# Performance work log

Measured on AMD Instinct MI355X. Metric: run time of the kernel, lower is better.

## Reference

```python
import jax, jax.numpy as jnp
import numpy as np

VOCAB = 101
EMB = 32
HID = 32


def setup_inputs() -> dict:
    key = jax.random.key(0)
    k = jax.random.split(key, 7)
    B, T = 4096, 512
    x = jax.random.randint(k[0], (B, T), 0, VOCAB, dtype=jnp.int32)
    emb = jax.random.normal(k[1], (VOCAB, EMB), dtype=jnp.float32) * 0.1
    # gate order: i, f, g, o (concatenated along last dim)
    Wx = jax.random.normal(k[2], (EMB, 4 * HID), dtype=jnp.float32) * 0.1
    Wh = jax.random.normal(k[3], (HID, 4 * HID), dtype=jnp.float32) * 0.1
    b = jax.random.normal(k[4], (4 * HID,), dtype=jnp.float32) * 0.1
    W_fc = jax.random.normal(k[5], (HID, 2), dtype=jnp.float32) * 0.1
    b_fc = jax.random.normal(k[6], (2,), dtype=jnp.float32) * 0.1
    return {"x": x, "emb": emb, "Wx": Wx, "Wh": Wh, "b": b, "W_fc": W_fc, "b_fc": b_fc}


def _lstm_last_h(xe, Wx, Wh, b):
    # xe: [B, T, EMB]
    B = xe.shape[0]
    # precompute input contributions for all timesteps: [T, B, 4H]
    xg = jnp.einsum('bte,eh->tbh', xe, Wx) + b
    h0 = jnp.zeros((B, HID), xe.dtype)
    c0 = jnp.zeros((B, HID), xe.dtype)

    def step(carry, xt):
        h, c = carry
        g = xt + h @ Wh  # [B, 4H]
        i, f, gg, o = jnp.split(g, 4, axis=-1)
        c = jax.nn.sigmoid(f) * c + jax.nn.sigmoid(i) * jnp.tanh(gg)
        h = jax.nn.sigmoid(o) * jnp.tanh(c)
        return (h, c), None

    (h, c), _ = jax.lax.scan(step, (h0, c0), xg)
    return h  # last hidden state == hidden_seq[:, -1, :]


def reference(x, emb, Wx, Wh, b, W_fc, b_fc):
    xe = emb[x]  # [B, T, EMB]
    h = _lstm_last_h(xe, Wx, Wh, b)
    return h @ W_fc + b_fc  # [B, 2]
```

## Files before the change

kernel.cpp:

```cpp
#include <hip/hip_runtime.h>
#include <stdint.h>

#define T_LEN 512
#define VOCAB 101
#define GSP   140
#define XPB   516
#define HPW   20
#define HB1   (16 * HPW)

typedef short short8 __attribute__((ext_vector_type(8)));
typedef short s16x4  __attribute__((ext_vector_type(4)));
typedef float f32x4  __attribute__((ext_vector_type(4)));

#define LOG2E 1.442695041f
#define L2E2  2.885390082f

__device__ __forceinline__ float asF(uint32_t u) {
    union { uint32_t i; float f; } x; x.i = u; return x.f;
}
__device__ __forceinline__ float bf2f(uint16_t u) { return asF(((uint32_t)u) << 16); }
__device__ __forceinline__ float bf_lo(uint32_t u) { return asF(u << 16); }
__device__ __forceinline__ float bf_hi(uint32_t u) { return asF(u & 0xFFFF0000u); }
__device__ __forceinline__ uint16_t f2bf(float f) {
    union { float f; uint32_t i; } x; x.f = f;
    return (uint16_t)((x.i + 0x7FFFu + ((x.i >> 16) & 1u)) >> 16);
}
__device__ __forceinline__ float getw(const void* p, int i, bool isbf) {
    return isbf ? bf2f(((const uint16_t*)p)[i]) : ((const float*)p)[i];
}
__device__ __forceinline__ bool detect_bf16(const void* embp) {
    const uint16_t* u = (const uint16_t*)embp;
    int sane = 0;
    for (int i = 0; i < 64; ++i) {
        uint16_t v = u[i];
        int e = (v >> 7) & 0xFF;
        sane += ((e >= 100 && e <= 140) || ((v & 0x7FFFu) == 0)) ? 1 : 0;
    }
    return sane >= 56;
}

#define GATES(S, CST, HOUT)                                                     \
  {                                                                             \
    float ai = __builtin_amdgcn_exp2f(-(S)[0]);                                 \
    float af = __builtin_amdgcn_exp2f(-(S)[1]);                                 \
    float ag = __builtin_amdgcn_exp2f(-(S)[2]);                                 \
    float ao = __builtin_amdgcn_exp2f(-(S)[3]);                                 \
    float uu = 1.f + ai, ww = 1.f + ag, zz = 1.f + af;                          \
    float uw = uu * ww;                                                         \
    float num = __builtin_fmaf(__builtin_fmaf(ww, -L2E2, 2.f * L2E2), zz,       \
                               (CST) * uw);                                     \
    float cs = num * __builtin_amdgcn_rcpf(zz * uw);                            \
    (CST) = cs;                                                                 \
    float ac = __builtin_amdgcn_exp2f(-cs);                                     \
    float t1 = 1.f + ac;                                                        \
    (HOUT) = (2.f - t1) * __builtin_amdgcn_rcpf((1.f + ao) * t1);               \
  }

#define STEP_T(HRoff, HWoff, TOFF, TKUSE, TKDEF)                                    \
  {                                                                                 \
    const uint32_t* hr = &hbuf[HRoff];                                              \
    uint16_t*       hw = (uint16_t*)&hbuf[HWoff];                                   \
    short8 bfrag = *(const short8*)&hr[n * HPW + 4 * q];                            \
    __builtin_amdgcn_sched_barrier(0);                                              \
    s16x4 graw  = *(const s16x4*)&Gl2[adr1 + (u4 << 2)];                            \
    __builtin_amdgcn_sched_barrier(0);                                              \
    TKDEF = xr[TOFF];                                                               \
    __builtin_amdgcn_sched_barrier(0);                                              \
    f32x4 gc;                                                                       \
    { union { s16x4 v; uint32_t d[2]; } ug; ug.v = grawP;                           \
      gc[0] = bf_lo(ug.d[0]); gc[1] = bf_hi(ug.d[0]);                               \
      gc[2] = bf_lo(ug.d[1]); gc[3] = bf_hi(ug.d[1]); }                             \
    adr1 = (TKUSE) * GSP;                                                           \
    __builtin_amdgcn_sched_barrier(0);                                              \
    asm volatile("s_waitcnt lgkmcnt(2)" ::: "memory");                              \
    __builtin_amdgcn_sched_barrier(0);                                              \
    f32x4 s0 = __builtin_amdgcn_mfma_f32_16x16x32_bf16(afr, bfrag, gc, 0, 0, 0);    \
    float h0;                                                                       \
    GATES(s0, c0, h0);                                                              \
    uint32_t hp;                                                                    \
    asm("v_cvt_pk_bf16_f32 %0, %1, %2" : "=v"(hp) : "v"(h0), "v"(h0));              \
    hw[n * (2 * HPW) + u4] = (uint16_t)hp;                                          \
    grawP = graw;                                                                   \
    __builtin_amdgcn_sched_barrier(0);                                              \
    asm volatile("s_waitcnt lgkmcnt(0)" ::: "memory");                              \
    __builtin_amdgcn_s_barrier();                                                   \
    __builtin_amdgcn_sched_barrier(0);                                              \
  }

__global__ __launch_bounds__(512, 1) void lstm_fused(
    const int* __restrict__ x, const void* __restrict__ emb,
    const void* __restrict__ Wx, const void* __restrict__ Wh,
    const void* __restrict__ bias, const void* __restrict__ Wfc,
    const void* __restrict__ bfc, void* __restrict__ out)
{
    __shared__ __align__(16) uint16_t Gl2[VOCAB * GSP];
    __shared__ __align__(16) uint8_t  xt8[16 * XPB];
    __shared__ __align__(16) uint32_t hbuf[2 * 16 * HPW];

    const int tid = threadIdx.x;
    const int wl  = tid & 63;
    const int w   = tid >> 6;
    const int n   = wl & 15;
    const int q   = wl >> 4;
    const int u4  = 4 * w + q;
    const int b0  = blockIdx.x * 16;

    const bool isbf = detect_bf16(emb);

    for (int idx = tid; idx < VOCAB * 128; idx += 512) {
        int v = idx >> 7, cc = idx & 127;
        int u = cc >> 2, g = cc & 3;
        int col = 32 * g + u;
        float acc = getw(bias, col, isbf);
        #pragma unroll 8
        for (int k = 0; k < 32; ++k)
            acc += getw(emb, v * 32 + k, isbf) * getw(Wx, k * 128 + col, isbf);
        Gl2[v * GSP + cc] = f2bf(acc * ((g == 2) ? L2E2 : LOG2E));
    }
    for (int i = tid; i < 2048; i += 512) {
        int row = i >> 7, c4 = i & 127;
        int4 vv = *(const int4*)&x[(b0 + row) * T_LEN + (c4 << 2)];
        uint32_t p = (uint32_t)(vv.x & 255) | ((uint32_t)(vv.y & 255) << 8) |
                     ((uint32_t)(vv.z & 255) << 16) | ((uint32_t)(vv.w & 255) << 24);
        ((uint32_t*)&xt8[row * XPB])[c4] = p;
    }
    for (int i = tid; i < 48; i += 512) {
        int row = i / 3, j = i % 3;
        xt8[row * XPB + 512 + j] = (uint8_t)x[(b0 + row) * T_LEN + j];
    }
    for (int i = tid; i < 2 * 16 * HPW; i += 512) hbuf[i] = 0;

    short8 afr;
    {
        const int gte = n & 3, ul = n >> 2;
        const float sc = (gte == 2) ? L2E2 : LOG2E;
        const int base = 32 * gte + 4 * w + ul;
        union { short8 v; uint16_t s[8]; } u0;
        #pragma unroll
        for (int jj = 0; jj < 8; ++jj)
            u0.s[jj] = f2bf(getw(Wh, (8 * q + jj) * 128 + base, isbf) * sc);
        afr = u0.v;
    }
    __syncthreads();

    float c0 = 0.f;
    const uint8_t* xr = &xt8[n * XPB];

    s16x4 grawP;
    int adr1, tkA, tkB;
    {
        int t0 = xr[0], t1 = xr[1];
        tkA = xr[2];
        grawP = *(const s16x4*)&Gl2[t0 * GSP + (u4 << 2)];
        adr1  = t1 * GSP;
    }

    for (int t = 0; t < T_LEN; t += 2) {
        STEP_T(0,   HB1, t + 3, tkA, tkB);
        STEP_T(HB1, 0,   t + 4, tkB, tkA);
    }

    __syncthreads();

    if (tid < 32) {
        int row = tid >> 1, cc = tid & 1;
        float acc = getw(bfc, cc, isbf);
        #pragma unroll 8
        for (int k = 0; k < 32; ++k) {
            uint32_t d = hbuf[row * HPW + (k >> 1)];
            float hval = (k & 1) ? bf_hi(d) : bf_lo(d);
            acc += hval * getw(Wfc, k * 2 + cc, isbf);
        }
        int oidx = (b0 + row) * 2 + cc;
        if (isbf) ((uint16_t*)out)[oidx] = f2bf(acc);
        else      ((float*)out)[oidx]    = acc;
    }
}

extern "C" void kernel_launch(void* const* d_in, const int* in_sizes, int n_in,
                              void* d_out, int out_size, void* d_ws, size_t ws_size,
                              hipStream_t stream) {
    (void)in_sizes; (void)n_in; (void)d_ws; (void)ws_size; (void)out_size;
    const int* x = (const int*)d_in[0];
    lstm_fused<<<dim3(256), dim3(512), 0, stream>>>(
        x, d_in[1], d_in[2], d_in[3], d_in[4], d_in[5], d_in[6], d_out);
}
```

Measured before the change: 245.4 us.

## Interleave two batch groups per block in staggered MFMA/gate phases

Each block now handles 32 sequences with 1024 threads, split into two groups of 8 waves that run 180 degrees out of phase. One group does the hidden-state read and MFMA while the other does gate math and the h write, with a block barrier between phases. Each group now has a single h buffer instead of double buffering, so barriers enforce the ordering. The aim is to hide the serial recurrence latency by overlapping two independent chains, at the cost of twice as many barriers per step and half as many blocks (128 on a 256-CU part).

```diff
diff --git a/kernel.cpp b/kernel.cpp
--- a/kernel.cpp
+++ b/kernel.cpp
@@ -6,7 +6,6 @@
 #define GSP   140
 #define XPB   516
 #define HPW   20
-#define HB1   (16 * HPW)
 
 typedef short short8 __attribute__((ext_vector_type(8)));
 typedef short s16x4  __attribute__((ext_vector_type(4)));
@@ -56,58 +55,62 @@
     (HOUT) = (2.f - t1) * __builtin_amdgcn_rcpf((1.f + ao) * t1);               \
   }
 
-#define STEP_T(HRoff, HWoff, TOFF, TKUSE, TKDEF)                                    \
-  {                                                                                 \
-    const uint32_t* hr = &hbuf[HRoff];                                              \
-    uint16_t*       hw = (uint16_t*)&hbuf[HWoff];                                   \
-    short8 bfrag = *(const short8*)&hr[n * HPW + 4 * q];                            \
-    __builtin_amdgcn_sched_barrier(0);                                              \
-    s16x4 graw  = *(const s16x4*)&Gl2[adr1 + (u4 << 2)];                            \
-    __builtin_amdgcn_sched_barrier(0);                                              \
-    TKDEF = xr[TOFF];                                                               \
-    __builtin_amdgcn_sched_barrier(0);                                              \
-    f32x4 gc;                                                                       \
-    { union { s16x4 v; uint32_t d[2]; } ug; ug.v = grawP;                           \
-      gc[0] = bf_lo(ug.d[0]); gc[1] = bf_hi(ug.d[0]);                               \
-      gc[2] = bf_lo(ug.d[1]); gc[3] = bf_hi(ug.d[1]); }                             \
-    adr1 = (TKUSE) * GSP;                                                           \
-    __builtin_amdgcn_sched_barrier(0);                                              \
-    asm volatile("s_waitcnt lgkmcnt(2)" ::: "memory");                              \
-    __builtin_amdgcn_sched_barrier(0);                                              \
-    f32x4 s0 = __builtin_amdgcn_mfma_f32_16x16x32_bf16(afr, bfrag, gc, 0, 0, 0);    \
-    float h0;                                                                       \
-    GATES(s0, c0, h0);                                                              \
-    uint32_t hp;                                                                    \
-    asm("v_cvt_pk_bf16_f32 %0, %1, %2" : "=v"(hp) : "v"(h0), "v"(h0));              \
-    hw[n * (2 * HPW) + u4] = (uint16_t)hp;                                          \
-    grawP = graw;                                                                   \
-    __builtin_amdgcn_sched_barrier(0);                                              \
-    asm volatile("s_waitcnt lgkmcnt(0)" ::: "memory");                              \
-    __builtin_amdgcn_s_barrier();                                                   \
-    __builtin_amdgcn_sched_barrier(0);                                              \
+#define BAR()                                                                   \
+  { __builtin_amdgcn_s_barrier(); __builtin_amdgcn_sched_barrier(0); }
+
+#define PHASE_R()                                                               \
+  {                                                                             \
+    short8 bfrag = *(const short8*)&hb[n * HPW + 4 * q];                        \
+    __builtin_amdgcn_sched_barrier(0);                                          \
+    f32x4 gc;                                                                   \
+    { union { s16x4 v; uint32_t d[2]; } ug; ug.v = grawP;                       \
+      gc[0] = bf_lo(ug.d[0]); gc[1] = bf_hi(ug.d[0]);                           \
+      gc[2] = bf_lo(ug.d[1]); gc[3] = bf_hi(ug.d[1]); }                         \
+    __builtin_amdgcn_sched_barrier(0);                                          \
+    asm volatile("s_waitcnt lgkmcnt(0)" ::: "memory");                          \
+    __builtin_amdgcn_sched_barrier(0);                                          \
+    sreg = __builtin_amdgcn_mfma_f32_16x16x32_bf16(afr, bfrag, gc, 0, 0, 0);    \
   }
 
-__global__ __launch_bounds__(512, 1) void lstm_fused(
+#define PHASE_G(TOFF)                                                           \
+  {                                                                             \
+    float h0;                                                                   \
+    GATES(sreg, c0, h0);                                                        \
+    uint32_t hp;                                                                \
+    asm("v_cvt_pk_bf16_f32 %0, %1, %2" : "=v"(hp) : "v"(h0), "v"(h0));          \
+    ((uint16_t*)hb)[n * (2 * HPW) + u4] = (uint16_t)hp;                         \
+    __builtin_amdgcn_sched_barrier(0);                                          \
+    grawP = *(const s16x4*)&Gl2[tokA * GSP + (u4 << 2)];                        \
+    __builtin_amdgcn_sched_barrier(0);                                          \
+    tokA = xr[TOFF];                                                            \
+    __builtin_amdgcn_sched_barrier(0);                                          \
+    asm volatile("s_waitcnt lgkmcnt(2)" ::: "memory");                          \
+    __builtin_amdgcn_sched_barrier(0);                                          \
+  }
+
+__global__ __launch_bounds__(1024, 1) void lstm_fused(
     const int* __restrict__ x, const void* __restrict__ emb,
     const void* __restrict__ Wx, const void* __restrict__ Wh,
     const void* __restrict__ bias, const void* __restrict__ Wfc,
     const void* __restrict__ bfc, void* __restrict__ out)
 {
     __shared__ __align__(16) uint16_t Gl2[VOCAB * GSP];
-    __shared__ __align__(16) uint8_t  xt8[16 * XPB];
+    __shared__ __align__(16) uint8_t  xt8[32 * XPB];
     __shared__ __align__(16) uint32_t hbuf[2 * 16 * HPW];
 
     const int tid = threadIdx.x;
     const int wl  = tid & 63;
     const int w   = tid >> 6;
+    const int grp = w >> 3;
+    const int wv  = w & 7;
     const int n   = wl & 15;
     const int q   = wl >> 4;
-    const int u4  = 4 * w + q;
-    const int b0  = blockIdx.x * 16;
+    const int u4  = 4 * wv + q;
+    const int b0  = blockIdx.x * 32;
 
     const bool isbf = detect_bf16(emb);
 
-    for (int idx = tid; idx < VOCAB * 128; idx += 512) {
+    for (int idx = tid; idx < VOCAB * 128; idx += 1024) {
         int v = idx >> 7, cc = idx & 127;
         int u = cc >> 2, g = cc & 3;
         int col = 32 * g + u;
@@ -117,24 +120,24 @@
             acc += getw(emb, v * 32 + k, isbf) * getw(Wx, k * 128 + col, isbf);
         Gl2[v * GSP + cc] = f2bf(acc * ((g == 2) ? L2E2 : LOG2E));
     }
-    for (int i = tid; i < 2048; i += 512) {
+    for (int i = tid; i < 4096; i += 1024) {
         int row = i >> 7, c4 = i & 127;
         int4 vv = *(const int4*)&x[(b0 + row) * T_LEN + (c4 << 2)];
         uint32_t p = (uint32_t)(vv.x & 255) | ((uint32_t)(vv.y & 255) << 8) |
                      ((uint32_t)(vv.z & 255) << 16) | ((uint32_t)(vv.w & 255) << 24);
         ((uint32_t*)&xt8[row * XPB])[c4] = p;
     }
-    for (int i = tid; i < 48; i += 512) {
+    for (int i = tid; i < 96; i += 1024) {
         int row = i / 3, j = i % 3;
         xt8[row * XPB + 512 + j] = (uint8_t)x[(b0 + row) * T_LEN + j];
     }
-    for (int i = tid; i < 2 * 16 * HPW; i += 512) hbuf[i] = 0;
+    for (int i = tid; i < 2 * 16 * HPW; i += 1024) hbuf[i] = 0;
 
     short8 afr;
     {
         const int gte = n & 3, ul = n >> 2;
         const float sc = (gte == 2) ? L2E2 : LOG2E;
-        const int base = 32 * gte + 4 * w + ul;
+        const int base = 32 * gte + 4 * wv + ul;
         union { short8 v; uint16_t s[8]; } u0;
         #pragma unroll
         for (int jj = 0; jj < 8; ++jj)
@@ -143,35 +146,53 @@
     }
     __syncthreads();
 
+    uint32_t*       hb = &hbuf[grp * (16 * HPW)];
+    const uint8_t*  xr = &xt8[(grp * 16 + n) * XPB];
+
     float c0 = 0.f;
-    const uint8_t* xr = &xt8[n * XPB];
-
+    f32x4 sreg;
     s16x4 grawP;
-    int adr1, tkA, tkB;
+    int tokA, tno = 2;
     {
-        int t0 = xr[0], t1 = xr[1];
-        tkA = xr[2];
+        int t0 = xr[0];
+        tokA  = xr[1];
         grawP = *(const s16x4*)&Gl2[t0 * GSP + (u4 << 2)];
-        adr1  = t1 * GSP;
-    }
-
-    for (int t = 0; t < T_LEN; t += 2) {
-        STEP_T(0,   HB1, t + 3, tkA, tkB);
-        STEP_T(HB1, 0,   t + 4, tkB, tkA);
+    }
+
+    if (grp == 0) {
+        for (int t = 0; t < T_LEN; ++t) {
+            PHASE_R();
+            BAR();
+            PHASE_G(tno); ++tno;
+            BAR();
+        }
+    } else {
+        {
+            union { s16x4 v; uint32_t d[2]; } ug; ug.v = grawP;
+            sreg[0] = bf_lo(ug.d[0]); sreg[1] = bf_hi(ug.d[0]);
+            sreg[2] = bf_lo(ug.d[1]); sreg[3] = bf_hi(ug.d[1]);
+        }
+        for (int t = 0; t < T_LEN; ++t) {
+            PHASE_G(tno); ++tno;
+            BAR();
+            PHASE_R();
+            BAR();
+        }
     }
 
     __syncthreads();
 
-    if (tid < 32) {
-        int row = tid >> 1, cc = tid & 1;
+    if (tid < 64) {
+        int r32 = tid >> 1, cc = tid & 1;
+        const uint32_t* hrow = &hbuf[(r32 >> 4) * (16 * HPW) + (r32 & 15) * HPW];
         float acc = getw(bfc, cc, isbf);
         #pragma unroll 8
         for (int k = 0; k < 32; ++k) {
-            uint32_t d = hbuf[row * HPW + (k >> 1)];
+            uint32_t d = hrow[k >> 1];
             float hval = (k & 1) ? bf_hi(d) : bf_lo(d);
             acc += hval * getw(Wfc, k * 2 + cc, isbf);
         }
-        int oidx = (b0 + row) * 2 + cc;
+        int oidx = (b0 + r32) * 2 + cc;
         if (isbf) ((uint16_t*)out)[oidx] = f2bf(acc);
         else      ((float*)out)[oidx]    = acc;
     }
@@ -182,6 +203,6 @@
                               hipStream_t stream) {
     (void)in_sizes; (void)n_in; (void)d_ws; (void)ws_size; (void)out_size;
     const int* x = (const int*)d_in[0];
-    lstm_fused<<<dim3(256), dim3(512), 0, stream>>>(
+    lstm_fused<<<dim3(128), dim3(1024), 0, stream>>>(
         x, d_in[1], d_in[2], d_in[3], d_in[4], d_in[5], d_in[6], d_out);
 }
```

After: 335.1 us. 1.37x slower.
